# Optimization experiments

Measured on AMD Instinct MI355X. Metric: run time of the kernel, lower is better.

The kernel has to match this reference:

```python
import jax, jax.numpy as jnp
import numpy as np

WS = 16                     # window_size
OW = 24                     # overlap_win_size = int(16*0.5)+16
PAD = (OW - WS) // 2        # unfold padding = 4
DIM = 384
HEADS = 6
HID = 768                   # mlp_ratio 2.0 * dim
TABLE = (WS + OW - 1) ** 2  # 1521


def _rel_pos_index():
    ch = np.arange(WS)
    coords = np.stack(np.meshgrid(ch, ch, indexing='ij')).reshape(2, -1)      # (2, WS*WS)
    co = np.arange(OW)
    coords_o = np.stack(np.meshgrid(co, co, indexing='ij')).reshape(2, -1)    # (2, OW*OW)
    rel = coords[:, :, None] - coords_o[:, None, :]                           # (2, nq, nk)
    rel = rel.transpose(1, 2, 0).astype(np.int64)
    rel[..., 0] += OW - 1
    rel[..., 1] += OW - 1
    rel[..., 0] *= WS + OW - 1
    return rel.sum(-1)                                                        # (WS*WS, OW*OW)

RPI = jnp.asarray(_rel_pos_index())


def _ln(x, g, b, eps=1e-5):
    m = x.mean(-1, keepdims=True)
    v = ((x - m) ** 2).mean(-1, keepdims=True)
    return (x - m) / jnp.sqrt(v + eps) * g + b


def _overlap_windows(t, H, W):
    # t: (B,H,W,C) -> (B*nw, OW*OW, C); overlapping patches, stride WS, pad PAD
    B, _, _, C = t.shape
    nH, nW = H // WS, W // WS
    tp = jnp.pad(t, ((0, 0), (PAD, PAD), (PAD, PAD), (0, 0)))
    r = (jnp.arange(nH) * WS)[:, None] + jnp.arange(OW)   # (nH, OW)
    c = (jnp.arange(nW) * WS)[:, None] + jnp.arange(OW)   # (nW, OW)
    p = tp[:, r]              # (B, nH, OW, Wp, C)
    p = p[:, :, :, c]         # (B, nH, OW, nW, OW, C)
    p = p.transpose(0, 1, 3, 2, 4, 5).reshape(B * nH * nW, OW * OW, C)
    return p


def setup_inputs() -> dict:
    key = jax.random.key(0)
    ks = jax.random.split(key, 8)
    H = W = 192
    B = 1
    inp = {
        'x': jax.random.normal(ks[0], (B, H * W, DIM), dtype=jnp.float32),
        'norm1_g': jnp.ones((DIM,), jnp.float32),
        'norm1_b': jnp.zeros((DIM,), jnp.float32),
        'qkv_w': jax.random.normal(ks[1], (DIM, 3 * DIM), jnp.float32) * 0.02,
        'qkv_b': jnp.zeros((3 * DIM,), jnp.float32),
        'rpb_table': jax.random.normal(ks[2], (TABLE, HEADS), jnp.float32) * 0.02,
        'proj_w': jax.random.normal(ks[3], (DIM, DIM), jnp.float32) * 0.02,
        'proj_b': jnp.zeros((DIM,), jnp.float32),
        'norm2_g': jnp.ones((DIM,), jnp.float32),
        'norm2_b': jnp.zeros((DIM,), jnp.float32),
        'fc1_w': jax.random.normal(ks[4], (DIM, HID), jnp.float32) * 0.02,
        'fc1_b': jnp.zeros((HID,), jnp.float32),
        'fc2_w': jax.random.normal(ks[5], (HID, DIM), jnp.float32) * 0.02,
        'fc2_b': jnp.zeros((DIM,), jnp.float32),
        'H': H,
        'W': W,
    }
    return inp


def reference(x, norm1_g, norm1_b, qkv_w, qkv_b, rpb_table, proj_w, proj_b,
              norm2_g, norm2_b, fc1_w, fc1_b, fc2_w, fc2_b, H, W):
    B, L, C = x.shape
    d = C // HEADS
    scale = d ** (-0.5)
    nH, nW = H // WS, W // WS

    shortcut = x
    xn = _ln(x, norm1_g, norm1_b).reshape(B, H, W, C)
    qkv = xn @ qkv_w + qkv_b                                   # (B,H,W,3C)
    q, k, v = qkv[..., :C], qkv[..., C:2 * C], qkv[..., 2 * C:]

    # non-overlapping query windows: (B*nw, WS*WS, C)
    qw = q.reshape(B, nH, WS, nW, WS, C).transpose(0, 1, 3, 2, 4, 5).reshape(-1, WS * WS, C)
    # overlapping key/value windows: (B*nw, OW*OW, C)
    kw = _overlap_windows(k, H, W)
    vw = _overlap_windows(v, H, W)

    b_ = qw.shape[0]
    qh = qw.reshape(b_, WS * WS, HEADS, d) * scale
    kh = kw.reshape(b_, OW * OW, HEADS, d)
    vh = vw.reshape(b_, OW * OW, HEADS, d)

    attn = jnp.einsum('bqhd,bkhd->bhqk', qh, kh)               # (b_, H, nq, nk)
    bias = rpb_table[RPI].transpose(2, 0, 1)                   # (heads, nq, nk)
    attn = jax.nn.softmax(attn + bias[None], axis=-1)
    out = jnp.einsum('bhqk,bkhd->bqhd', attn, vh).reshape(b_, WS * WS, C)

    # window reverse -> (B, H*W, C)
    out = out.reshape(B, nH, nW, WS, WS, C).transpose(0, 1, 3, 2, 4, 5).reshape(B, H * W, C)
    out = out @ proj_w + proj_b

    x = shortcut + out
    h = _ln(x, norm2_g, norm2_b)
    h = jax.nn.gelu(h @ fc1_w + fc1_b, approximate=False)
    h = h @ fc2_w + fc2_b
    return x + h
```

## Files before the change

kernel.cpp:

```cpp
#include <hip/hip_runtime.h>

#define LTOK 36864
#define DIMC 384
#define NHEADS 6
#define HDIM 64
#define HIDD 768
#define NWIN 12
#define WSZ 16
#define OWS 24
#define KVTOK 576

using bf16x8 = __attribute__((ext_vector_type(8))) short;
using f32x4  = __attribute__((ext_vector_type(4))) float;

__device__ inline unsigned short f2bf(float f) {
  unsigned u = __float_as_uint(f);
  return (unsigned short)((u + 0x7FFFu + ((u >> 16) & 1u)) >> 16);
}
__device__ __forceinline__ unsigned cvt_pk_bf16(float lo, float hi) {
  unsigned r;
  asm volatile("v_cvt_pk_bf16_f32 %0, %1, %2" : "=v"(r) : "v"(lo), "v"(hi));
  return r;
}
__device__ __forceinline__ unsigned short f2bf1(float x) {
  return (unsigned short)(cvt_pk_bf16(x, x) & 0xffffu);
}
__device__ __forceinline__ float fexp2(float x) {
#if __has_builtin(__builtin_amdgcn_exp2f)
  return __builtin_amdgcn_exp2f(x);
#else
  return exp2f(x);
#endif
}

typedef __attribute__((address_space(1))) const unsigned int GAS_U32;
typedef __attribute__((address_space(3))) unsigned int LAS_U32;
__device__ __forceinline__ void gl16(const void* g, void* l) {
  __builtin_amdgcn_global_load_lds((GAS_U32*)g, (LAS_U32*)l, 16, 0, 0);
}

__global__ void convt_kernel(const float* __restrict__ w, unsigned short* __restrict__ wt,
                             int K, int N) {
  int id = blockIdx.x * 256 + threadIdx.x;
  if (id >= K * N) return;
  int n = id / K;
  int k = id - n * K;
  wt[id] = f2bf(w[(size_t)k * N + n]);
}

__global__ void rpb_expand_kernel(const float* __restrict__ rpb, float* __restrict__ biasm8) {
  int id = blockIdx.x * 256 + threadIdx.x;
  if (id >= NHEADS * 256 * 576) return;
  int head = id / 147456;
  int rem = id - head * 147456;
  int q = rem / 576;
  int kt = rem - q * 576;
  int ty = q >> 4, tx = q & 15;
  int oy = kt / 24, ox = kt - (kt / 24) * 24;
  biasm8[id] = rpb[((ty - oy + 23) * 39 + (tx - ox + 23)) * NHEADS + head] * 8.0f;
}

__global__ __launch_bounds__(256) void ln_kernel(const float* __restrict__ x,
                                                 const float* __restrict__ g,
                                                 const float* __restrict__ b,
                                                 unsigned short* __restrict__ out) {
  int row = blockIdx.x * 4 + (threadIdx.x >> 6);
  int lane = threadIdx.x & 63;
  const float* xr = x + (size_t)row * DIMC;
  float v[6];
  float s = 0.f, ss = 0.f;
#pragma unroll
  for (int i = 0; i < 6; ++i) {
    v[i] = xr[lane + i * 64];
    s += v[i];
    ss += v[i] * v[i];
  }
#pragma unroll
  for (int off = 32; off; off >>= 1) {
    s += __shfl_xor(s, off);
    ss += __shfl_xor(ss, off);
  }
  float mean = s * (1.f / DIMC);
  float var = ss * (1.f / DIMC) - mean * mean;
  float rstd = rsqrtf(var + 1e-5f);
  unsigned short* outr = out + (size_t)row * DIMC;
#pragma unroll
  for (int i = 0; i < 6; ++i) {
    int c = lane + i * 64;
    outr[c] = f2bf((v[i] - mean) * rstd * g[c] + b[c]);
  }
}

template <int EPI>
__global__ __launch_bounds__(256) void gemm_bf16(const unsigned short* __restrict__ A,
                                                 const unsigned short* __restrict__ Bt,
                                                 const float* __restrict__ bias,
                                                 const float* __restrict__ resid,
                                                 void* __restrict__ outv,
                                                 int M, int N, int K) {
  __shared__ unsigned short As[2][4096];
  __shared__ unsigned short Bs[2][4096];
  const int tid = threadIdx.x;
  int id = blockIdx.y * gridDim.x + blockIdx.x;
  int chunk = (gridDim.x * gridDim.y) >> 3;
  int lid = (id & 7) * chunk + (id >> 3);
  const int m0 = (lid / gridDim.x) * 128;
  const int n0 = (lid % gridDim.x) * 128;
  const int lane = tid & 63;
  const int wave = tid >> 6;
  const int wr = wave >> 1;
  const int wc = wave & 1;
  const int l15 = lane & 15, l4 = lane >> 4;

  f32x4 acc[4][4];
#pragma unroll
  for (int i = 0; i < 4; ++i)
#pragma unroll
    for (int j = 0; j < 4; ++j) acc[i][j] = (f32x4){0.f, 0.f, 0.f, 0.f};

  const int srow = tid >> 2;
  const int scol = (tid & 3) << 3;
  const unsigned short* ga = A + (size_t)(m0 + srow) * K + scol;
  const unsigned short* gb = Bt + (size_t)(n0 + srow) * K + scol;

#define STAGE(buf, k0)                                        \
  do {                                                        \
    unsigned short* lA = As[buf] + wave * 512;                \
    unsigned short* lB = Bs[buf] + wave * 512;                \
    gl16(ga + (k0), lA);                                      \
    gl16(ga + (size_t)64 * K + (k0), lA + 2048);              \
    gl16(gb + (k0), lB);                                      \
    gl16(gb + (size_t)64 * K + (k0), lB + 2048);              \
  } while (0)

  STAGE(0, 0);
  __syncthreads();

  const int nt = K >> 5;
  for (int t = 0; t < nt; ++t) {
    const int cur = t & 1;
    if (t + 1 < nt) STAGE(cur ^ 1, (t + 1) * 32);

    const unsigned short* arp = As[cur] + (wr * 64 + l15) * 32 + l4 * 8;
    const unsigned short* brp = Bs[cur] + (wc * 64 + l15) * 32 + l4 * 8;
    bf16x8 af[4], bfr[4];
#pragma unroll
    for (int i = 0; i < 4; ++i) af[i] = *(const bf16x8*)(arp + i * 512);
#pragma unroll
    for (int j = 0; j < 4; ++j) bfr[j] = *(const bf16x8*)(brp + j * 512);
#pragma unroll
    for (int i = 0; i < 4; ++i)
#pragma unroll
      for (int j = 0; j < 4; ++j)
        acc[i][j] = __builtin_amdgcn_mfma_f32_16x16x32_bf16(af[i], bfr[j], acc[i][j], 0, 0, 0);

    __syncthreads();
  }
#undef STAGE

#pragma unroll
  for (int j = 0; j < 4; ++j) {
    int gcol = n0 + wc * 64 + j * 16 + l15;
    float bv = bias[gcol];
#pragma unroll
    for (int i = 0; i < 4; ++i) {
#pragma unroll
      for (int r = 0; r < 4; ++r) {
        int grow = m0 + wr * 64 + i * 16 + l4 * 4 + r;
        float v = acc[i][j][r] + bv;
        size_t idx = (size_t)grow * N + gcol;
        if (EPI == 0) {
          ((unsigned short*)outv)[idx] = f2bf(v);
        } else if (EPI == 1) {
          ((float*)outv)[idx] = resid[idx] + v;
        } else {
          float gv = 0.5f * v * (1.f + erff(v * 0.70710678118654752f));
          ((unsigned short*)outv)[idx] = f2bf(gv);
        }
      }
    }
  }
}

__global__ __launch_bounds__(256, 3) void attn_kernel(const unsigned short* __restrict__ qkv,
                                                      const float* __restrict__ biasm8,
                                                      unsigned short* __restrict__ att) {
  __shared__ unsigned short ks[64][72];
  __shared__ unsigned short vts[64][72];
  __shared__ unsigned short pt[4][32][40];
  int bid = blockIdx.x;
  int lid = (bid & 7) * 216 + (bid >> 3);
  const int hw = lid >> 1;
  const int qh = lid & 1;
  const int win = hw / NHEADS;
  const int head = hw - win * NHEADS;
  const int wy = win / NWIN, wx = win - (win / NWIN) * NWIN;
  const int tid = threadIdx.x;
  const int w = tid >> 6, lane = tid & 63;
  const int l15 = lane & 15, l4 = lane >> 4;
  const float SC02 = 0.125f * 1.44269504f;
  const float C0 = -8.f * 1.44269504f;

  const int qrow0 = qh * 128 + w * 32;

  bf16x8 qf[2][2];
#pragma unroll
  for (int jq = 0; jq < 2; ++jq) {
    int q = qrow0 + jq * 16 + l15;
    int gy = wy * WSZ + (q >> 4), gx = wx * WSZ + (q & 15);
    const unsigned short* qp = qkv + (size_t)(gy * 192 + gx) * 1152 + head * HDIM + l4 * 8;
    qf[jq][0] = *(const bf16x8*)qp;
    qf[jq][1] = *(const bf16x8*)(qp + 32);
  }

  const float* bias_base = biasm8 + (size_t)head * 147456 + (size_t)(qrow0 + l15) * 576 + l4 * 4;

  {
    int kt = lane;
    int oy = kt / OWS, ox = kt - (kt / OWS) * OWS;
    int gy = wy * WSZ + oy - 4, gx = wx * WSZ + ox - 4;
    uint4 k0 = {0,0,0,0}, k1 = {0,0,0,0}, v0 = {0,0,0,0}, v1 = {0,0,0,0};
    if ((unsigned)gy < 192u && (unsigned)gx < 192u) {
      const unsigned short* gp = qkv + (size_t)(gy * 192 + gx) * 1152 + DIMC + head * HDIM + w * 16;
      k0 = *(const uint4*)gp;         k1 = *(const uint4*)(gp + 8);
      v0 = *(const uint4*)(gp + 384); v1 = *(const uint4*)(gp + 392);
    }
    *(uint4*)&ks[lane][w * 16]     = k0;
    *(uint4*)&ks[lane][w * 16 + 8] = k1;
    const unsigned short* vv = (const unsigned short*)&v0;
#pragma unroll
    for (int j = 0; j < 8; ++j) vts[w * 16 + j][lane] = vv[j];
    vv = (const unsigned short*)&v1;
#pragma unroll
    for (int j = 0; j < 8; ++j) vts[w * 16 + 8 + j][lane] = vv[j];
  }
  __syncthreads();

  f32x4 oacc[2][4];
#pragma unroll
  for (int i = 0; i < 2; ++i)
#pragma unroll
    for (int j = 0; j < 4; ++j) oacc[i][j] = (f32x4){0.f, 0.f, 0.f, 0.f};
  float plsum[2] = {0.f, 0.f};

  for (int kb = 0; kb < 9; ++kb) {
    const bool have = kb < 8;
    uint4 pk0 = {0,0,0,0}, pk1 = {0,0,0,0}, pv0 = {0,0,0,0}, pv1 = {0,0,0,0};
    if (have) {
      int kt = (kb + 1) * 64 + lane;
      int oy = kt / OWS, ox = kt - (kt / OWS) * OWS;
      int gy = wy * WSZ + oy - 4, gx = wx * WSZ + ox - 4;
      if ((unsigned)gy < 192u && (unsigned)gx < 192u) {
        const unsigned short* gp = qkv + (size_t)(gy * 192 + gx) * 1152 + DIMC + head * HDIM + w * 16;
        pk0 = *(const uint4*)gp;         pk1 = *(const uint4*)(gp + 8);
        pv0 = *(const uint4*)(gp + 384); pv1 = *(const uint4*)(gp + 392);
      }
    }

    f32x4 sacc[4][2];
    const float* bp = bias_base + kb * 64;
#pragma unroll
    for (int i = 0; i < 4; ++i)
#pragma unroll
      for (int j2 = 0; j2 < 2; ++j2)
        sacc[i][j2] = *(const f32x4*)(bp + j2 * (16 * 576) + i * 16);
#pragma unroll
    for (int kk = 0; kk < 2; ++kk) {
      bf16x8 kf[4];
#pragma unroll
      for (int i = 0; i < 4; ++i)
        kf[i] = *(const bf16x8*)&ks[i * 16 + l15][kk * 32 + l4 * 8];
      __builtin_amdgcn_s_setprio(1);
#pragma unroll
      for (int i = 0; i < 4; ++i)
#pragma unroll
        for (int j2 = 0; j2 < 2; ++j2)
          sacc[i][j2] = __builtin_amdgcn_mfma_f32_16x16x32_bf16(kf[i], qf[j2][kk], sacc[i][j2], 0, 0, 0);
      __builtin_amdgcn_s_setprio(0);
    }

#pragma unroll
    for (int i = 0; i < 4; ++i)
#pragma unroll
      for (int j2 = 0; j2 < 2; ++j2)
#pragma unroll
        for (int r = 0; r < 4; ++r) {
          float p = fexp2(fmaf(sacc[i][j2][r], SC02, C0));
          sacc[i][j2][r] = p;
          plsum[j2] += p;
        }

#pragma unroll
    for (int kk = 0; kk < 2; ++kk) {
#pragma unroll
      for (int i2 = 0; i2 < 2; ++i2)
#pragma unroll
        for (int j2 = 0; j2 < 2; ++j2) {
          int i = kk * 2 + i2;
          uint2 pk;
          pk.x = cvt_pk_bf16(sacc[i][j2][0], sacc[i][j2][1]);
          pk.y = cvt_pk_bf16(sacc[i][j2][2], sacc[i][j2][3]);
          *(uint2*)&pt[w][j2 * 16 + l15][i2 * 16 + l4 * 4] = pk;
        }
      bf16x8 pf[2], vf[4];
#pragma unroll
      for (int j2 = 0; j2 < 2; ++j2)
        pf[j2] = *(const bf16x8*)&pt[w][j2 * 16 + l15][l4 * 8];
#pragma unroll
      for (int jd = 0; jd < 4; ++jd)
        vf[jd] = *(const bf16x8*)&vts[jd * 16 + l15][kk * 32 + l4 * 8];
      __builtin_amdgcn_s_setprio(1);
#pragma unroll
      for (int j2 = 0; j2 < 2; ++j2)
#pragma unroll
        for (int jd = 0; jd < 4; ++jd)
          oacc[j2][jd] = __builtin_amdgcn_mfma_f32_16x16x32_bf16(pf[j2], vf[jd], oacc[j2][jd], 0, 0, 0);
      __builtin_amdgcn_s_setprio(0);
    }

    if (have) {
      __syncthreads();
      *(uint4*)&ks[lane][w * 16]     = pk0;
      *(uint4*)&ks[lane][w * 16 + 8] = pk1;
      const unsigned short* vv = (const unsigned short*)&pv0;
#pragma unroll
      for (int j = 0; j < 8; ++j) vts[w * 16 + j][lane] = vv[j];
      vv = (const unsigned short*)&pv1;
#pragma unroll
      for (int j = 0; j < 8; ++j) vts[w * 16 + 8 + j][lane] = vv[j];
      __syncthreads();
    }
  }

  float invl[2];
#pragma unroll
  for (int j2 = 0; j2 < 2; ++j2) {
    plsum[j2] += __shfl_xor(plsum[j2], 16);
    plsum[j2] += __shfl_xor(plsum[j2], 32);
    invl[j2] = 1.f / plsum[j2];
  }

#pragma unroll
  for (int j2 = 0; j2 < 2; ++j2) {
#pragma unroll
    for (int r = 0; r < 4; ++r) {
      float il = __shfl(invl[j2], l4 * 4 + r);
      int q = qrow0 + j2 * 16 + l4 * 4 + r;
      int gy = wy * WSZ + (q >> 4), gx = wx * WSZ + (q & 15);
      unsigned short* op = att + (size_t)(gy * 192 + gx) * DIMC + head * HDIM + l15;
#pragma unroll
      for (int jd = 0; jd < 4; ++jd) op[jd * 16] = f2bf1(oacc[j2][jd][r] * il);
    }
  }
}

extern "C" void kernel_launch(void* const* d_in, const int* in_sizes, int n_in,
                              void* d_out, int out_size, void* d_ws, size_t ws_size,
                              hipStream_t stream) {
  const float* x      = (const float*)d_in[0];
  const float* n1g    = (const float*)d_in[1];
  const float* n1b    = (const float*)d_in[2];
  const float* qkv_w  = (const float*)d_in[3];
  const float* qkv_b  = (const float*)d_in[4];
  const float* rpb    = (const float*)d_in[5];
  const float* proj_w = (const float*)d_in[6];
  const float* proj_b = (const float*)d_in[7];
  const float* n2g    = (const float*)d_in[8];
  const float* n2b    = (const float*)d_in[9];
  const float* fc1_w  = (const float*)d_in[10];
  const float* fc1_b  = (const float*)d_in[11];
  const float* fc2_w  = (const float*)d_in[12];
  const float* fc2_b  = (const float*)d_in[13];
  float* out = (float*)d_out;

  char* ws = (char*)d_ws;
  unsigned short* xn   = (unsigned short*)ws;
  unsigned short* qkvb = (unsigned short*)(ws + 28311552);
  unsigned short* att  = (unsigned short*)(ws + 28311552 + 84934656);
  unsigned short* wq   = (unsigned short*)(ws + 141557760);
  unsigned short* wp   = wq + 1152 * 384;
  unsigned short* w1   = wp + 384 * 384;
  unsigned short* w2   = w1 + 768 * 384;
  float* biasm8 = (float*)ws;

  convt_kernel<<<(DIMC * 3 * DIMC + 255) / 256, 256, 0, stream>>>(qkv_w, wq, DIMC, 3 * DIMC);
  convt_kernel<<<(DIMC * DIMC + 255) / 256, 256, 0, stream>>>(proj_w, wp, DIMC, DIMC);
  convt_kernel<<<(DIMC * HIDD + 255) / 256, 256, 0, stream>>>(fc1_w, w1, DIMC, HIDD);
  convt_kernel<<<(HIDD * DIMC + 255) / 256, 256, 0, stream>>>(fc2_w, w2, HIDD, DIMC);

  ln_kernel<<<LTOK / 4, 256, 0, stream>>>(x, n1g, n1b, xn);
  gemm_bf16<0><<<dim3(1152 / 128, LTOK / 128), 256, 0, stream>>>(xn, wq, qkv_b, nullptr, qkvb,
                                                                 LTOK, 1152, DIMC);
  rpb_expand_kernel<<<(NHEADS * 256 * 576 + 255) / 256, 256, 0, stream>>>(rpb, biasm8);
  attn_kernel<<<dim3(NHEADS * 144 * 2), 256, 0, stream>>>(qkvb, biasm8, att);
  gemm_bf16<1><<<dim3(DIMC / 128, LTOK / 128), 256, 0, stream>>>(att, wp, proj_b, x, out,
                                                                 LTOK, DIMC, DIMC);
  ln_kernel<<<LTOK / 4, 256, 0, stream>>>(out, n2g, n2b, xn);
  gemm_bf16<2><<<dim3(HIDD / 128, LTOK / 128), 256, 0, stream>>>(xn, w1, fc1_b, nullptr, qkvb,
                                                                 LTOK, HIDD, DIMC);
  gemm_bf16<1><<<dim3(DIMC / 128, LTOK / 128), 256, 0, stream>>>(qkvb, w2, fc2_b, out, out,
                                                                 LTOK, DIMC, HIDD);
}
```

Measured before the change: 339.1 us.

## Deepen GEMM LDS pipeline to four stages with swizzled layout; swizzle attention K/V LDS

The GEMM moves from a double-buffered LDS pipeline with two barriers per k-step to a four-buffer ring. Three tiles are prefetched, gated by vmcnt waits, and only one barrier is taken per iteration. The global-to-LDS staging and fragment reads now use an XOR-swizzled row layout meant to avoid LDS bank conflicts. The attention kernel replaces its padded K and V^T shared arrays with unpadded XOR-swizzled layouts, which cuts LDS footprint and keeps reads conflict-free. In exchange, GEMM LDS use doubles, which may lower occupancy, and the tail clamps prefetch addresses, issuing redundant loads.

```diff
diff --git a/kernel.cpp b/kernel.cpp
--- a/kernel.cpp
+++ b/kernel.cpp
@@ -98,8 +98,8 @@
                                                  const float* __restrict__ resid,
                                                  void* __restrict__ outv,
                                                  int M, int N, int K) {
-  __shared__ unsigned short As[2][4096];
-  __shared__ unsigned short Bs[2][4096];
+  __shared__ unsigned short As[4][4096];
+  __shared__ unsigned short Bs[4][4096];
   const int tid = threadIdx.x;
   int id = blockIdx.y * gridDim.x + blockIdx.x;
   int chunk = (gridDim.x * gridDim.y) >> 3;
@@ -118,8 +118,11 @@
 #pragma unroll
     for (int j = 0; j < 4; ++j) acc[i][j] = (f32x4){0.f, 0.f, 0.f, 0.f};
 
-  const int srow = tid >> 2;
-  const int scol = (tid & 3) << 3;
+  {
+  }
+  const int sl = (tid & 7) ^ ((tid >> 3) & 7);
+  const int srow = 2 * (tid >> 3) + (sl >> 2);
+  const int scol = (sl & 3) << 3;
   const unsigned short* ga = A + (size_t)(m0 + srow) * K + scol;
   const unsigned short* gb = Bt + (size_t)(n0 + srow) * K + scol;
 
@@ -133,30 +136,41 @@
     gl16(gb + (size_t)64 * K + (k0), lB + 2048);              \
   } while (0)
 
+  const int nt = K >> 5;
   STAGE(0, 0);
-  __syncthreads();
-
-  const int nt = K >> 5;
+  STAGE(1, 32);
+  STAGE(2, 64);
+
+  const int fswz = ((((l15 & 1) << 2) + l4) ^ (l15 >> 1)) << 4;
+  const int abase = (wr * 32 + (l15 >> 1)) * 128 + fswz;
+  const int bbase = (wc * 32 + (l15 >> 1)) * 128 + fswz;
+
   for (int t = 0; t < nt; ++t) {
-    const int cur = t & 1;
-    if (t + 1 < nt) STAGE(cur ^ 1, (t + 1) * 32);
-
-    const unsigned short* arp = As[cur] + (wr * 64 + l15) * 32 + l4 * 8;
-    const unsigned short* brp = Bs[cur] + (wc * 64 + l15) * 32 + l4 * 8;
+    const int cur = t & 3;
+    asm volatile("s_waitcnt vmcnt(8)" ::: "memory");
+    __builtin_amdgcn_s_barrier();
+
+    {
+      int kc = (t + 3) * 32;
+      if (kc > K - 32) kc = K - 32;
+      STAGE((t + 3) & 3, kc);
+    }
+
+    const char* arp = (const char*)As[cur] + abase;
+    const char* brp = (const char*)Bs[cur] + bbase;
     bf16x8 af[4], bfr[4];
 #pragma unroll
-    for (int i = 0; i < 4; ++i) af[i] = *(const bf16x8*)(arp + i * 512);
-#pragma unroll
-    for (int j = 0; j < 4; ++j) bfr[j] = *(const bf16x8*)(brp + j * 512);
+    for (int i = 0; i < 4; ++i) af[i] = *(const bf16x8*)(arp + i * 1024);
+#pragma unroll
+    for (int j = 0; j < 4; ++j) bfr[j] = *(const bf16x8*)(brp + j * 1024);
 #pragma unroll
     for (int i = 0; i < 4; ++i)
 #pragma unroll
       for (int j = 0; j < 4; ++j)
         acc[i][j] = __builtin_amdgcn_mfma_f32_16x16x32_bf16(af[i], bfr[j], acc[i][j], 0, 0, 0);
-
-    __syncthreads();
   }
 #undef STAGE
+  asm volatile("s_waitcnt vmcnt(0)" ::: "memory");
 
 #pragma unroll
   for (int j = 0; j < 4; ++j) {
@@ -185,8 +199,8 @@
 __global__ __launch_bounds__(256, 3) void attn_kernel(const unsigned short* __restrict__ qkv,
                                                       const float* __restrict__ biasm8,
                                                       unsigned short* __restrict__ att) {
-  __shared__ unsigned short ks[64][72];
-  __shared__ unsigned short vts[64][72];
+  __shared__ unsigned short ks[64 * 64];
+  __shared__ unsigned short vts[64 * 64];
   __shared__ unsigned short pt[4][32][40];
   int bid = blockIdx.x;
   int lid = (bid & 7) * 216 + (bid >> 3);
@@ -215,6 +229,27 @@
 
   const float* bias_base = biasm8 + (size_t)head * 147456 + (size_t)(qrow0 + l15) * 576 + l4 * 4;
 
+#define KS_W(kt, k0v, k1v)                                                             \
+  do {                                                                                 \
+    char* kb = (char*)ks + (kt) * 128;                                                 \
+    int sw = ((kt) & 7) << 4;                                                          \
+    *(uint4*)(kb + ((w * 32) ^ sw)) = (k0v);                                           \
+    *(uint4*)(kb + ((w * 32 + 16) ^ sw)) = (k1v);                                      \
+  } while (0)
+#define VTS_W(v0v, v1v)                                                                \
+  do {                                                                                 \
+    const unsigned short* vv = (const unsigned short*)&(v0v);                          \
+    _Pragma("unroll") for (int j = 0; j < 8; ++j) {                                    \
+      int d = w * 16 + j;                                                              \
+      *(unsigned short*)((char*)vts + d * 128 + (((lane * 2)) ^ ((j & 7) << 4))) = vv[j]; \
+    }                                                                                  \
+    vv = (const unsigned short*)&(v1v);                                                \
+    _Pragma("unroll") for (int j = 0; j < 8; ++j) {                                    \
+      int d = w * 16 + 8 + j;                                                          \
+      *(unsigned short*)((char*)vts + d * 128 + (((lane * 2)) ^ ((j & 7) << 4))) = vv[j]; \
+    }                                                                                  \
+  } while (0)
+
   {
     int kt = lane;
     int oy = kt / OWS, ox = kt - (kt / OWS) * OWS;
@@ -225,14 +260,8 @@
       k0 = *(const uint4*)gp;         k1 = *(const uint4*)(gp + 8);
       v0 = *(const uint4*)(gp + 384); v1 = *(const uint4*)(gp + 392);
     }
-    *(uint4*)&ks[lane][w * 16]     = k0;
-    *(uint4*)&ks[lane][w * 16 + 8] = k1;
-    const unsigned short* vv = (const unsigned short*)&v0;
-#pragma unroll
-    for (int j = 0; j < 8; ++j) vts[w * 16 + j][lane] = vv[j];
-    vv = (const unsigned short*)&v1;
-#pragma unroll
-    for (int j = 0; j < 8; ++j) vts[w * 16 + 8 + j][lane] = vv[j];
+    KS_W(lane, k0, k1);
+    VTS_W(v0, v1);
   }
   __syncthreads();
 
@@ -242,6 +271,8 @@
 #pragma unroll
     for (int j = 0; j < 4; ++j) oacc[i][j] = (f32x4){0.f, 0.f, 0.f, 0.f};
   float plsum[2] = {0.f, 0.f};
+
+  const int rsw = (l15 & 7) << 4;
 
   for (int kb = 0; kb < 9; ++kb) {
     const bool have = kb < 8;
@@ -269,7 +300,7 @@
       bf16x8 kf[4];
 #pragma unroll
       for (int i = 0; i < 4; ++i)
-        kf[i] = *(const bf16x8*)&ks[i * 16 + l15][kk * 32 + l4 * 8];
+        kf[i] = *(const bf16x8*)((char*)ks + (i * 16 + l15) * 128 + ((kk * 64 + l4 * 16) ^ rsw));
       __builtin_amdgcn_s_setprio(1);
 #pragma unroll
       for (int i = 0; i < 4; ++i)
@@ -308,7 +339,7 @@
         pf[j2] = *(const bf16x8*)&pt[w][j2 * 16 + l15][l4 * 8];
 #pragma unroll
       for (int jd = 0; jd < 4; ++jd)
-        vf[jd] = *(const bf16x8*)&vts[jd * 16 + l15][kk * 32 + l4 * 8];
+        vf[jd] = *(const bf16x8*)((char*)vts + (jd * 16 + l15) * 128 + ((kk * 64 + l4 * 16) ^ rsw));
       __builtin_amdgcn_s_setprio(1);
 #pragma unroll
       for (int j2 = 0; j2 < 2; ++j2)
@@ -320,17 +351,13 @@
 
     if (have) {
       __syncthreads();
-      *(uint4*)&ks[lane][w * 16]     = pk0;
-      *(uint4*)&ks[lane][w * 16 + 8] = pk1;
-      const unsigned short* vv = (const unsigned short*)&pv0;
-#pragma unroll
-      for (int j = 0; j < 8; ++j) vts[w * 16 + j][lane] = vv[j];
-      vv = (const unsigned short*)&pv1;
-#pragma unroll
-      for (int j = 0; j < 8; ++j) vts[w * 16 + 8 + j][lane] = vv[j];
+      KS_W(lane, pk0, pk1);
+      VTS_W(pv0, pv1);
       __syncthreads();
     }
   }
+#undef KS_W
+#undef VTS_W
 
   float invl[2];
 #pragma unroll
```

After: 366.3 us. +8.0%, slower.

## Store GEMM and attention LDS tiles in MFMA fragment order to avoid bank conflicts

Applied to the files above, without the earlier changes.

Reorders the shared-memory layout of the GEMM A/B tiles and the attention K and V^T tiles so that each lane's 16-byte MFMA fragment sits at a contiguous lane*16 offset. Global-to-LDS staging addresses are remapped to match, and the padded 72-wide arrays become flat buffers. The aim is conflict-free, linear ds_read_b128 fragment loads. The V transpose scatter still writes 2-byte elements, so write-side bank conflicts may change.

```diff
diff --git a/kernel.cpp b/kernel.cpp
--- a/kernel.cpp
+++ b/kernel.cpp
@@ -118,10 +118,8 @@
 #pragma unroll
     for (int j = 0; j < 4; ++j) acc[i][j] = (f32x4){0.f, 0.f, 0.f, 0.f};
 
-  const int srow = tid >> 2;
-  const int scol = (tid & 3) << 3;
-  const unsigned short* ga = A + (size_t)(m0 + srow) * K + scol;
-  const unsigned short* gb = Bt + (size_t)(n0 + srow) * K + scol;
+  const unsigned short* ga = A + (size_t)(m0 + wave * 16 + l15) * K + l4 * 8;
+  const unsigned short* gb = Bt + (size_t)(n0 + wave * 16 + l15) * K + l4 * 8;
 
 #define STAGE(buf, k0)                                        \
   do {                                                        \
@@ -141,13 +139,13 @@
     const int cur = t & 1;
     if (t + 1 < nt) STAGE(cur ^ 1, (t + 1) * 32);
 
-    const unsigned short* arp = As[cur] + (wr * 64 + l15) * 32 + l4 * 8;
-    const unsigned short* brp = Bs[cur] + (wc * 64 + l15) * 32 + l4 * 8;
+    const char* ab = (const char*)As[cur] + wr * 4096 + lane * 16;
+    const char* bb = (const char*)Bs[cur] + wc * 4096 + lane * 16;
     bf16x8 af[4], bfr[4];
 #pragma unroll
-    for (int i = 0; i < 4; ++i) af[i] = *(const bf16x8*)(arp + i * 512);
-#pragma unroll
-    for (int j = 0; j < 4; ++j) bfr[j] = *(const bf16x8*)(brp + j * 512);
+    for (int i = 0; i < 4; ++i) af[i] = *(const bf16x8*)(ab + i * 1024);
+#pragma unroll
+    for (int j = 0; j < 4; ++j) bfr[j] = *(const bf16x8*)(bb + j * 1024);
 #pragma unroll
     for (int i = 0; i < 4; ++i)
 #pragma unroll
@@ -185,8 +183,8 @@
 __global__ __launch_bounds__(256, 3) void attn_kernel(const unsigned short* __restrict__ qkv,
                                                       const float* __restrict__ biasm8,
                                                       unsigned short* __restrict__ att) {
-  __shared__ unsigned short ks[64][72];
-  __shared__ unsigned short vts[64][72];
+  __shared__ unsigned short ks[4096];
+  __shared__ unsigned short vts[4096];
   __shared__ unsigned short pt[4][32][40];
   int bid = blockIdx.x;
   int lid = (bid & 7) * 216 + (bid >> 3);
@@ -215,6 +213,23 @@
 
   const float* bias_base = biasm8 + (size_t)head * 147456 + (size_t)(qrow0 + l15) * 576 + l4 * 4;
 
+#define KS_W(k0v, k1v)                                                     \
+  do {                                                                     \
+    char* kb = (char*)ks + (lane >> 4) * 2048 + (lane & 15) * 16;          \
+    *(uint4*)(kb + (2 * w) * 256) = (k0v);                                 \
+    *(uint4*)(kb + (2 * w + 1) * 256) = (k1v);                             \
+  } while (0)
+#define VTS_W(v0v, v1v)                                                    \
+  do {                                                                     \
+    char* vb = (char*)vts + w * 2048 + (lane >> 3) * 256 + (lane & 7) * 2; \
+    const unsigned short* vv = (const unsigned short*)&(v0v);              \
+    _Pragma("unroll") for (int j = 0; j < 8; ++j)                          \
+        *(unsigned short*)(vb + j * 16) = vv[j];                           \
+    vv = (const unsigned short*)&(v1v);                                    \
+    _Pragma("unroll") for (int j = 0; j < 8; ++j)                          \
+        *(unsigned short*)(vb + 128 + j * 16) = vv[j];                     \
+  } while (0)
+
   {
     int kt = lane;
     int oy = kt / OWS, ox = kt - (kt / OWS) * OWS;
@@ -225,14 +240,8 @@
       k0 = *(const uint4*)gp;         k1 = *(const uint4*)(gp + 8);
       v0 = *(const uint4*)(gp + 384); v1 = *(const uint4*)(gp + 392);
     }
-    *(uint4*)&ks[lane][w * 16]     = k0;
-    *(uint4*)&ks[lane][w * 16 + 8] = k1;
-    const unsigned short* vv = (const unsigned short*)&v0;
-#pragma unroll
-    for (int j = 0; j < 8; ++j) vts[w * 16 + j][lane] = vv[j];
-    vv = (const unsigned short*)&v1;
-#pragma unroll
-    for (int j = 0; j < 8; ++j) vts[w * 16 + 8 + j][lane] = vv[j];
+    KS_W(k0, k1);
+    VTS_W(v0, v1);
   }
   __syncthreads();
 
@@ -269,7 +278,7 @@
       bf16x8 kf[4];
 #pragma unroll
       for (int i = 0; i < 4; ++i)
-        kf[i] = *(const bf16x8*)&ks[i * 16 + l15][kk * 32 + l4 * 8];
+        kf[i] = *(const bf16x8*)((const char*)ks + i * 2048 + kk * 1024 + lane * 16);
       __builtin_amdgcn_s_setprio(1);
 #pragma unroll
       for (int i = 0; i < 4; ++i)
@@ -308,7 +317,7 @@
         pf[j2] = *(const bf16x8*)&pt[w][j2 * 16 + l15][l4 * 8];
 #pragma unroll
       for (int jd = 0; jd < 4; ++jd)
-        vf[jd] = *(const bf16x8*)&vts[jd * 16 + l15][kk * 32 + l4 * 8];
+        vf[jd] = *(const bf16x8*)((const char*)vts + jd * 2048 + kk * 1024 + lane * 16);
       __builtin_amdgcn_s_setprio(1);
 #pragma unroll
       for (int j2 = 0; j2 < 2; ++j2)
@@ -320,17 +329,13 @@
 
     if (have) {
       __syncthreads();
-      *(uint4*)&ks[lane][w * 16]     = pk0;
-      *(uint4*)&ks[lane][w * 16 + 8] = pk1;
-      const unsigned short* vv = (const unsigned short*)&pv0;
-#pragma unroll
-      for (int j = 0; j < 8; ++j) vts[w * 16 + j][lane] = vv[j];
-      vv = (const unsigned short*)&pv1;
-#pragma unroll
-      for (int j = 0; j < 8; ++j) vts[w * 16 + 8 + j][lane] = vv[j];
+      KS_W(pk0, pk1);
+      VTS_W(pv0, pv1);
       __syncthreads();
     }
   }
+#undef KS_W
+#undef VTS_W
 
   float invl[2];
 #pragma unroll
```

Result: slower. 390.9 us (+15.3%).

## Double-buffer K/V shared tiles and prefetch next bias block in attention

Applied to the files above, without the earlier changes.

Turns the K and transposed-V shared-memory tiles into two-slot ping-pong buffers, so the next block's K/V are written into the other slot. This lets each iteration use one barrier instead of two. The bias loads that seed the score accumulators are also issued one iteration early, right after the next tile is stored, to hide their global latency. Shared memory use roughly doubles for K/V, which may lower occupancy below the three blocks per CU set in the launch bounds. The extra live registers for the prefetched bias may also add pressure.

```diff
diff --git a/kernel.cpp b/kernel.cpp
--- a/kernel.cpp
+++ b/kernel.cpp
@@ -185,8 +185,8 @@
 __global__ __launch_bounds__(256, 3) void attn_kernel(const unsigned short* __restrict__ qkv,
                                                       const float* __restrict__ biasm8,
                                                       unsigned short* __restrict__ att) {
-  __shared__ unsigned short ks[64][72];
-  __shared__ unsigned short vts[64][72];
+  __shared__ unsigned short ks[2][64][72];
+  __shared__ unsigned short vts[2][64][72];
   __shared__ unsigned short pt[4][32][40];
   int bid = blockIdx.x;
   int lid = (bid & 7) * 216 + (bid >> 3);
@@ -215,6 +215,21 @@
 
   const float* bias_base = biasm8 + (size_t)head * 147456 + (size_t)(qrow0 + l15) * 576 + l4 * 4;
 
+#define KS_W(buf, k0v, k1v)                          \
+  do {                                               \
+    *(uint4*)&ks[buf][lane][w * 16] = (k0v);         \
+    *(uint4*)&ks[buf][lane][w * 16 + 8] = (k1v);     \
+  } while (0)
+#define VTS_W(buf, v0v, v1v)                                           \
+  do {                                                                 \
+    const unsigned short* vv = (const unsigned short*)&(v0v);          \
+    _Pragma("unroll") for (int j = 0; j < 8; ++j)                      \
+        vts[buf][w * 16 + j][lane] = vv[j];                            \
+    vv = (const unsigned short*)&(v1v);                                \
+    _Pragma("unroll") for (int j = 0; j < 8; ++j)                      \
+        vts[buf][w * 16 + 8 + j][lane] = vv[j];                        \
+  } while (0)
+
   {
     int kt = lane;
     int oy = kt / OWS, ox = kt - (kt / OWS) * OWS;
@@ -225,15 +240,17 @@
       k0 = *(const uint4*)gp;         k1 = *(const uint4*)(gp + 8);
       v0 = *(const uint4*)(gp + 384); v1 = *(const uint4*)(gp + 392);
     }
-    *(uint4*)&ks[lane][w * 16]     = k0;
-    *(uint4*)&ks[lane][w * 16 + 8] = k1;
-    const unsigned short* vv = (const unsigned short*)&v0;
-#pragma unroll
-    for (int j = 0; j < 8; ++j) vts[w * 16 + j][lane] = vv[j];
-    vv = (const unsigned short*)&v1;
-#pragma unroll
-    for (int j = 0; j < 8; ++j) vts[w * 16 + 8 + j][lane] = vv[j];
-  }
+    KS_W(0, k0, k1);
+    VTS_W(0, v0, v1);
+  }
+
+  f32x4 sacc[4][2];
+#pragma unroll
+  for (int i = 0; i < 4; ++i)
+#pragma unroll
+    for (int j2 = 0; j2 < 2; ++j2)
+      sacc[i][j2] = *(const f32x4*)(bias_base + j2 * (16 * 576) + i * 16);
+
   __syncthreads();
 
   f32x4 oacc[2][4];
@@ -244,6 +261,7 @@
   float plsum[2] = {0.f, 0.f};
 
   for (int kb = 0; kb < 9; ++kb) {
+    const int cur = kb & 1;
     const bool have = kb < 8;
     uint4 pk0 = {0,0,0,0}, pk1 = {0,0,0,0}, pv0 = {0,0,0,0}, pv1 = {0,0,0,0};
     if (have) {
@@ -257,19 +275,12 @@
       }
     }
 
-    f32x4 sacc[4][2];
-    const float* bp = bias_base + kb * 64;
-#pragma unroll
-    for (int i = 0; i < 4; ++i)
-#pragma unroll
-      for (int j2 = 0; j2 < 2; ++j2)
-        sacc[i][j2] = *(const f32x4*)(bp + j2 * (16 * 576) + i * 16);
 #pragma unroll
     for (int kk = 0; kk < 2; ++kk) {
       bf16x8 kf[4];
 #pragma unroll
       for (int i = 0; i < 4; ++i)
-        kf[i] = *(const bf16x8*)&ks[i * 16 + l15][kk * 32 + l4 * 8];
+        kf[i] = *(const bf16x8*)&ks[cur][i * 16 + l15][kk * 32 + l4 * 8];
       __builtin_amdgcn_s_setprio(1);
 #pragma unroll
       for (int i = 0; i < 4; ++i)
@@ -308,7 +319,7 @@
         pf[j2] = *(const bf16x8*)&pt[w][j2 * 16 + l15][l4 * 8];
 #pragma unroll
       for (int jd = 0; jd < 4; ++jd)
-        vf[jd] = *(const bf16x8*)&vts[jd * 16 + l15][kk * 32 + l4 * 8];
+        vf[jd] = *(const bf16x8*)&vts[cur][jd * 16 + l15][kk * 32 + l4 * 8];
       __builtin_amdgcn_s_setprio(1);
 #pragma unroll
       for (int j2 = 0; j2 < 2; ++j2)
@@ -319,18 +330,19 @@
     }
 
     if (have) {
-      __syncthreads();
-      *(uint4*)&ks[lane][w * 16]     = pk0;
-      *(uint4*)&ks[lane][w * 16 + 8] = pk1;
-      const unsigned short* vv = (const unsigned short*)&pv0;
-#pragma unroll
-      for (int j = 0; j < 8; ++j) vts[w * 16 + j][lane] = vv[j];
-      vv = (const unsigned short*)&pv1;
-#pragma unroll
-      for (int j = 0; j < 8; ++j) vts[w * 16 + 8 + j][lane] = vv[j];
-      __syncthreads();
-    }
-  }
+      KS_W(cur ^ 1, pk0, pk1);
+      VTS_W(cur ^ 1, pv0, pv1);
+      const float* bp = bias_base + (kb + 1) * 64;
+#pragma unroll
+      for (int i = 0; i < 4; ++i)
+#pragma unroll
+        for (int j2 = 0; j2 < 2; ++j2)
+          sacc[i][j2] = *(const f32x4*)(bp + j2 * (16 * 576) + i * 16);
+    }
+    __syncthreads();
+  }
+#undef KS_W
+#undef VTS_W
 
   float invl[2];
 #pragma unroll
```

New measurement: 334.2 us. No clear change (-1.5%).
